# Performance work log

Measured on AMD Instinct MI355X. Metric: run time of the kernel, lower is better.

## Reference

```python
import jax, jax.numpy as jnp
import numpy as np

B, C, IC, H, W = 4, 256, 128, 64, 64
EPS = 1e-5  # BatchNorm eps (eval mode, running stats)


def conv_bn(x, w, b, gamma, beta, mean, var, relu):
    # 1x1 conv == channel contraction; BN in eval mode (affine w/ running stats)
    y = jnp.einsum('oc,bchw->bohw', w, x) + b[None, :, None, None]
    scale = gamma * jax.lax.rsqrt(var + EPS)
    shift = beta - mean * scale
    y = y * scale[None, :, None, None] + shift[None, :, None, None]
    return jax.nn.relu(y) if relu else y


def setup_inputs() -> dict:
    key = jax.random.key(0)
    ks = jax.random.split(key, 32)

    def branch(i, co, ci):
        return dict(
            w=jax.random.normal(ks[i], (co, ci), jnp.float32) * 0.05,
            b=jax.random.normal(ks[i + 1], (co,), jnp.float32) * 0.05,
            gamma=jax.random.uniform(ks[i + 2], (co,), jnp.float32, 0.5, 1.5),
            beta=jax.random.normal(ks[i + 3], (co,), jnp.float32) * 0.05,
            mean=jax.random.normal(ks[i + 4], (co,), jnp.float32) * 0.05,
            var=jax.random.uniform(ks[i + 5], (co,), jnp.float32, 0.5, 1.5),
        )

    g = branch(0, IC, C)
    th = branch(6, IC, C)
    ph = branch(12, IC, C)
    wo = branch(18, C, IC)
    inp = {'x': jax.random.normal(ks[24], (B, C, H, W), jnp.float32)}
    for pre, p in (('g', g), ('th', th), ('ph', ph), ('w', wo)):
        for k, v in p.items():
            inp[f'{pre}_{k}'] = v
    return inp


def reference(x, g_w, g_b, g_gamma, g_beta, g_mean, g_var,
              th_w, th_b, th_gamma, th_beta, th_mean, th_var,
              ph_w, ph_b, ph_gamma, ph_beta, ph_mean, ph_var,
              w_w, w_b, w_gamma, w_beta, w_mean, w_var):
    b, c, h, w = x.shape
    ic = g_w.shape[0]
    g_x = conv_bn(x, g_w, g_b, g_gamma, g_beta, g_mean, g_var, True).reshape(b, ic, h * w)     # [b,ic,n]
    theta = conv_bn(x, th_w, th_b, th_gamma, th_beta, th_mean, th_var, True).reshape(b, ic, h * w)
    phi = conv_bn(x, ph_w, ph_b, ph_gamma, ph_beta, ph_mean, ph_var, True).reshape(b, ic, h * w)
    # unscaled attention over flattened spatial positions
    f = jnp.einsum('bcn,bcm->bnm', theta, phi)     # [b,n,n]
    a = jax.nn.softmax(f, axis=2)
    y = jnp.einsum('bnm,bcm->bcn', a, g_x)         # [b,ic,n]
    y = y.reshape(b, ic, h, w)
    y = conv_bn(y, w_w, w_b, w_gamma, w_beta, w_mean, w_var, False)
    return y + x
```

## Files before the change

### kernel.cpp

```cpp
#include <hip/hip_runtime.h>
#include <math.h>

typedef __attribute__((ext_vector_type(8))) short short8;
typedef __attribute__((ext_vector_type(8))) _Float16 half8;
typedef __attribute__((ext_vector_type(4))) float f32x4;
typedef __attribute__((ext_vector_type(16))) float f32x16;

#define NSP 4096
#define CIN 256
#define ICH 128
#define SPLITS 4
#define TILES_PER_SPLIT 16
#define LOG2E 1.44269504088896f

__device__ __forceinline__ unsigned short f2h(float x){
  union { _Float16 h; unsigned short u; } v; v.h = (_Float16)x; return v.u;
}
__device__ __forceinline__ float h2f(unsigned short u){
  union { _Float16 h; unsigned short u; } v; v.u = u; return (float)v.h;
}
__device__ __forceinline__ unsigned pk2h(float a, float b){
  union { __fp16 __attribute__((ext_vector_type(2))) v; unsigned u; } r;
  r.v = __builtin_amdgcn_cvt_pkrtz(a, b);
  return r.u;
}
__device__ __forceinline__ float fexp2(float x){
  float r;
  asm("v_exp_f32 %0, %1" : "=v"(r) : "v"(x));
  return r;
}
__device__ __forceinline__ int swz(int row, int e){ return e ^ ((row & 7) << 3); }
__device__ __forceinline__ int swzK(int row, int e){ return e ^ ((row & 15) << 3); }

__device__ __forceinline__ f32x4 mfmah(short8 a, short8 b, f32x4 c){
  union { short8 s; half8 h; } ua, ub; ua.s = a; ub.s = b;
  return __builtin_amdgcn_mfma_f32_16x16x32_f16(ua.h, ub.h, c, 0, 0, 0);
}
__device__ __forceinline__ f32x16 mfma32(short8 a, short8 b, f32x16 c){
  union { short8 s; half8 h; } ua, ub; ua.s = a; ub.s = b;
  return __builtin_amdgcn_mfma_f32_32x32x16_f16(ua.h, ub.h, c, 0, 0, 0);
}

__device__ __forceinline__ void st4h(unsigned short* p, unsigned short a, unsigned short b,
                                     unsigned short c, unsigned short d){
  ushort4 v; v.x=a; v.y=b; v.z=c; v.w=d;
  *(ushort4*)p = v;
}

__device__ __forceinline__ void gload_lds16(const unsigned short* g, unsigned short* l){
  __builtin_amdgcn_global_load_lds(
      (const __attribute__((address_space(1))) unsigned int*)g,
      (__attribute__((address_space(3))) unsigned int*)l, 16, 0, 0);
}

__device__ __forceinline__ void stage_nc(const unsigned short* gbase, unsigned short* lds,
                                         int w, int l){
  #pragma unroll
  for (int i=0;i<4;++i){
    int rl = 16*w + 4*i + (l>>4);
    int eg = ((l&15)*8) ^ ((rl&15)<<3);
    gload_lds16(gbase + (size_t)rl*128 + eg, lds + w*2048 + i*512);
  }
}

__device__ __forceinline__ int kperm(int q){
  int m = q & 15;
  return (q & 16) | (((m>>2)&1)<<3) | (m&3) | (((m>>3)&1)<<2);
}

__global__ __launch_bounds__(256) void conv_fused_k(
    const float* __restrict__ x,
    const float* __restrict__ w0, const float* __restrict__ b0,
    const float* __restrict__ ga0, const float* __restrict__ be0,
    const float* __restrict__ me0, const float* __restrict__ va0,
    const float* __restrict__ w1, const float* __restrict__ b1,
    const float* __restrict__ ga1, const float* __restrict__ be1,
    const float* __restrict__ me1, const float* __restrict__ va1,
    const float* __restrict__ w2, const float* __restrict__ b2,
    const float* __restrict__ ga2, const float* __restrict__ be2,
    const float* __restrict__ me2, const float* __restrict__ va2,
    unsigned short* __restrict__ outg, unsigned short* __restrict__ outt,
    unsigned short* __restrict__ outp)
{
  const int b = blockIdx.z, nt = blockIdx.x, ot = blockIdx.y;
  const int n0 = nt*64, o0 = ot*64;
  const int t = threadIdx.x, w = t>>6, l = t&63;
  __shared__ unsigned short xs[64][64];
  __shared__ unsigned short ws[3][64][64];
  __shared__ float sc_s[3][64], sh_s[3][64];
  if (t < 64){
    int o = o0 + t;
    float s0 = ga0[o]*rsqrtf(va0[o]+1e-5f);
    sc_s[0][t]=s0; sh_s[0][t]=be0[o]-me0[o]*s0+b0[o]*s0;
    float s1 = ga1[o]*rsqrtf(va1[o]+1e-5f);
    sc_s[1][t]=s1*LOG2E; sh_s[1][t]=(be1[o]-me1[o]*s1+b1[o]*s1)*LOG2E;
    float s2 = ga2[o]*rsqrtf(va2[o]+1e-5f);
    sc_s[2][t]=s2; sh_s[2][t]=be2[o]-me2[o]*s2+b2[o]*s2;
  }
  const f32x4 Z = {0.f,0.f,0.f,0.f};
  f32x4 acc[3][4];
  #pragma unroll
  for (int br=0;br<3;++br) for (int i=0;i<4;++i) acc[br][i] = Z;
  const float* Wt[3] = {w0, w1, w2};

  for (int kc = 0; kc < CIN; kc += 64){
    __syncthreads();
    #pragma unroll
    for (int p = 0; p < 4; ++p){
      int cw = p*16 + (t>>4);
      int q4 = (t&15)*4;
      float4 xv = *(const float4*)(x + ((size_t)b*CIN + kc + cw)*NSP + n0 + q4);
      float xa[4] = {xv.x, xv.y, xv.z, xv.w};
      #pragma unroll
      for (int i=0;i<4;++i){
        int r = q4 + i;
        xs[r][swz(r, cw)] = f2h(xa[i]);
      }
      #pragma unroll
      for (int br=0;br<3;++br){
        float4 wv = *(const float4*)(Wt[br] + (size_t)(o0 + cw)*CIN + kc + q4);
        int cs = swz(cw, q4);
        st4h(&ws[br][cw][cs], f2h(wv.x), f2h(wv.y), f2h(wv.z), f2h(wv.w));
      }
    }
    __syncthreads();
    #pragma unroll
    for (int kf = 0; kf < 2; ++kf){
      int ko = kf*32 + (l>>4)*8;
      int wr = 16*w + (l&15);
      short8 wf0 = *(const short8*)&ws[0][wr][swz(wr, ko)];
      short8 wf1 = *(const short8*)&ws[1][wr][swz(wr, ko)];
      short8 wf2 = *(const short8*)&ws[2][wr][swz(wr, ko)];
      #pragma unroll
      for (int nf = 0; nf < 4; ++nf){
        int xr = 16*nf + (l&15);
        short8 xf = *(const short8*)&xs[xr][swz(xr, ko)];
        acc[0][nf] = mfmah(wf0, xf, acc[0][nf]);
        acc[1][nf] = mfmah(xf, wf1, acc[1][nf]);
        acc[2][nf] = mfmah(xf, wf2, acc[2][nf]);
      }
    }
  }
  #pragma unroll
  for (int j=0;j<4;++j){
    int ol = 16*w + (l>>4)*4 + j;
    float s = sc_s[0][ol], sh = sh_s[0][ol];
    #pragma unroll
    for (int nf=0;nf<4;++nf){
      int n = n0 + 16*nf + (l&15);
      int nst = (n & ~31) | kperm(n & 31);
      float v = fmaxf(acc[0][nf][j]*s + sh, 0.f);
      outg[((size_t)b*ICH + o0 + ol)*NSP + nst] = f2h(v);
    }
  }
  {
    int ol = 16*w + (l&15);
    float s1 = sc_s[1][ol], sh1 = sh_s[1][ol];
    float s2 = sc_s[2][ol], sh2 = sh_s[2][ol];
    #pragma unroll
    for (int nf=0; nf<4; ++nf)
      #pragma unroll
      for (int j=0;j<4;++j){
        int n = n0 + 16*nf + (l>>4)*4 + j;
        float v1 = fmaxf(acc[1][nf][j]*s1 + sh1, 0.f);
        float v2 = fmaxf(acc[2][nf][j]*s2 + sh2, 0.f);
        outt[((size_t)b*NSP + n)*ICH + o0 + ol] = f2h(v1);
        outp[((size_t)b*NSP + n)*ICH + o0 + ol] = f2h(v2);
      }
  }
}

__global__ __launch_bounds__(256, 2) void attn_k(
  const unsigned short* __restrict__ thp, const unsigned short* __restrict__ php,
  const unsigned short* __restrict__ gb, unsigned short* __restrict__ ypart,
  float* __restrict__ ml)
{
  const int bx = blockIdx.x;
  const int xcd = bx & 7, jj = bx >> 3;
  const int combo = xcd*2 + (jj>>5);
  const int qt = jj & 31;
  const int b = combo & 3, s = combo >> 2;
  const int n0 = qt*128;
  const int t = threadIdx.x, w = t>>6, l = t&63;
  const int hi = l>>5, ln = l&31;

  __shared__ unsigned short kb[2][8192];
  __shared__ unsigned short vb[2][8192];

  stage_nc(thp + ((size_t)b*NSP + n0      )*ICH, &kb[0][0], w, l);
  stage_nc(thp + ((size_t)b*NSP + n0 + 64 )*ICH, &kb[1][0], w, l);
  __syncthreads();
  short8 qf[8];
  {
    const unsigned short* qsrc = (w >> 1) ? &kb[1][0] : &kb[0][0];
    int r = 32*(w & 1) + ln;
    #pragma unroll
    for (int kc=0;kc<8;++kc)
      qf[kc] = *(const short8*)&qsrc[r*128 + swzK(r, kc*16 + 8*hi)];
  }
  __syncthreads();

  f32x16 oa[4];
  #pragma unroll
  for (int i=0;i<4;++i)
    #pragma unroll
    for (int j=0;j<16;++j) oa[i][j] = 0.f;
  float mr = -1e30f, lr = 0.f;
  unsigned pk[16];

  const int tile0 = s*TILES_PER_SPLIT;

  const unsigned short* kp[4];
  const unsigned short* vp[4];
  {
    const unsigned short* kbase = php + ((size_t)b*NSP + tile0*64)*ICH;
    const unsigned short* vbase = gb + (size_t)b*ICH*NSP + tile0*64;
    #pragma unroll
    for (int i=0;i<4;++i){
      int rl = 16*w + 4*i + (l>>4);
      int eg = ((l&15)*8) ^ ((rl&15)<<3);
      kp[i] = kbase + (size_t)rl*128 + eg;
      int cl = 32*w + 8*i + (l>>3);
      int me = ((l&7)*8) ^ ((cl&7)<<3);
      vp[i] = vbase + (size_t)cl*NSP + me;
    }
  }
  {
    unsigned short* kd = &kb[0][0] + w*2048;
    unsigned short* vd = &vb[0][0] + w*2048;
    #pragma unroll
    for (int i=0;i<4;++i){
      gload_lds16(kp[i], kd + i*512); kp[i] += 64*ICH;
      gload_lds16(vp[i], vd + i*512); vp[i] += 64;
    }
  }
  __syncthreads();
  int cur = 0;

  for (int it = 0; it < TILES_PER_SPLIT; ++it){
    if (it < TILES_PER_SPLIT-1){
      unsigned short* kd = &kb[cur^1][0] + w*2048;
      unsigned short* vd = &vb[cur^1][0] + w*2048;
      #pragma unroll
      for (int i=0;i<4;++i){
        gload_lds16(kp[i], kd + i*512); kp[i] += 64*ICH;
        gload_lds16(vp[i], vd + i*512); vp[i] += 64;
      }
    }

    f32x16 sc0, sc1;
    #pragma unroll
    for (int j=0;j<16;++j){ sc0[j]=0.f; sc1[j]=0.f; }
    __builtin_amdgcn_s_setprio(1);
    #pragma unroll
    for (int kc=0;kc<8;++kc){
      int eo = kc*16 + 8*hi;
      short8 a0 = *(const short8*)&kb[cur][(ln     )*128 + swzK(ln,      eo)];
      short8 a1 = *(const short8*)&kb[cur][(32 + ln)*128 + swzK(32 + ln, eo)];
      sc0 = mfma32(a0, qf[kc], sc0);
      sc1 = mfma32(a1, qf[kc], sc1);
    }
    __builtin_amdgcn_s_setprio(0);

    {
      float t0 = fmaxf(fmaxf(sc0[0],sc0[1]),  fmaxf(sc0[2],sc0[3]));
      float t1 = fmaxf(fmaxf(sc0[4],sc0[5]),  fmaxf(sc0[6],sc0[7]));
      float t2 = fmaxf(fmaxf(sc0[8],sc0[9]),  fmaxf(sc0[10],sc0[11]));
      float t3 = fmaxf(fmaxf(sc0[12],sc0[13]),fmaxf(sc0[14],sc0[15]));
      float t4 = fmaxf(fmaxf(sc1[0],sc1[1]),  fmaxf(sc1[2],sc1[3]));
      float t5 = fmaxf(fmaxf(sc1[4],sc1[5]),  fmaxf(sc1[6],sc1[7]));
      float t6 = fmaxf(fmaxf(sc1[8],sc1[9]),  fmaxf(sc1[10],sc1[11]));
      float t7 = fmaxf(fmaxf(sc1[12],sc1[13]),fmaxf(sc1[14],sc1[15]));
      float mx = fmaxf(fmaxf(fmaxf(t0,t1),fmaxf(t2,t3)),
                       fmaxf(fmaxf(t4,t5),fmaxf(t6,t7)));
      mx = fmaxf(mx, __shfl_xor(mx, 32));
      if (__any(mx - mr > 11.5f)){
        float mn = fmaxf(mr, mx);
        float al = fexp2(mr - mn);
        mr = mn; lr *= al;
        #pragma unroll
        for (int j=0;j<16;++j){
          int rowj = (j&3) + 8*(j>>2) + 4*hi;
          float alj = __shfl(al, rowj);
          #pragma unroll
          for (int ct=0;ct<4;++ct) oa[ct][j] *= alj;
        }
      }
      float sA=0.f, sB=0.f, sC=0.f, sD=0.f;
      #pragma unroll
      for (int r=0;r<16;r+=4){
        sc0[r]   = fexp2(sc0[r]  -mr); sA += sc0[r];
        sc0[r+1] = fexp2(sc0[r+1]-mr); sB += sc0[r+1];
        sc0[r+2] = fexp2(sc0[r+2]-mr); sC += sc0[r+2];
        sc0[r+3] = fexp2(sc0[r+3]-mr); sD += sc0[r+3];
      }
      #pragma unroll
      for (int r=0;r<16;r+=4){
        sc1[r]   = fexp2(sc1[r]  -mr); sA += sc1[r];
        sc1[r+1] = fexp2(sc1[r+1]-mr); sB += sc1[r+1];
        sc1[r+2] = fexp2(sc1[r+2]-mr); sC += sc1[r+2];
        sc1[r+3] = fexp2(sc1[r+3]-mr); sD += sc1[r+3];
      }
      lr += (sA + sB) + (sC + sD);
      #pragma unroll
      for (int s2=0;s2<2;++s2)
        #pragma unroll
        for (int q=0;q<4;++q){
          pk[s2*4+q]   = pk2h(sc0[8*s2+2*q], sc0[8*s2+2*q+1]);
          pk[8+s2*4+q] = pk2h(sc1[8*s2+2*q], sc1[8*s2+2*q+1]);
        }
    }

    __builtin_amdgcn_s_setprio(1);
    #pragma unroll
    for (int mt=0;mt<2;++mt)
      #pragma unroll
      for (int s2=0;s2<2;++s2){
        union { unsigned u[4]; short8 s8; } au;
        #pragma unroll
        for (int q=0;q<4;++q) au.u[q] = pk[8*mt+4*s2+q];
        int eo = 32*mt + 16*s2 + 8*hi;
        #pragma unroll
        for (int ct=0;ct<4;++ct){
          int cr = 32*ct + ln;
          short8 bv = *(const short8*)&vb[cur][cr*64 + swz(cr, eo)];
          oa[ct] = mfma32(au.s8, bv, oa[ct]);
        }
      }
    __builtin_amdgcn_s_setprio(0);

    __syncthreads();
    cur ^= 1;
  }

  lr += __shfl_xor(lr, 32);
  float invl = 1.f / lr;
  #pragma unroll
  for (int j=0;j<16;++j){
    int rowj = (j&3) + 8*(j>>2) + 4*hi;
    float invj = __shfl(invl, rowj);
    int n = n0 + 32*w + rowj;
    #pragma unroll
    for (int ct=0;ct<4;++ct){
      int c = 32*ct + ln;
      ypart[(((size_t)s*4 + b)*NSP + n)*ICH + c] = f2h(oa[ct][j]*invj);
    }
  }
  if (l < 32){
    int n = n0 + 32*w + l;
    ml[(((size_t)s*4 + b)*NSP + n)*2 + 0] = mr;
    ml[(((size_t)s*4 + b)*NSP + n)*2 + 1] = lr;
  }
}

__global__ __launch_bounds__(256) void final_k2(
  const unsigned short* __restrict__ ypart, const float* __restrict__ ml,
  const float* __restrict__ x, const float* __restrict__ Wm,
  const float* __restrict__ bias, const float* __restrict__ gamma,
  const float* __restrict__ beta, const float* __restrict__ mean,
  const float* __restrict__ var, float* __restrict__ out)
{
  const int b = blockIdx.z, oth = blockIdx.y, nt = blockIdx.x;
  const int n0 = nt*64, obase = oth*128;
  const int t = threadIdx.x, w = t>>6, l = t&63;
  __shared__ unsigned short ys[64][128];
  __shared__ unsigned short w2s[64][128];
  __shared__ float wc[SPLITS][64];
  __shared__ float sc_s[128], sh_s[128];
  if (t < 128){
    int o = obase + t;
    float s = gamma[o]*rsqrtf(var[o]+1e-5f);
    sc_s[t]=s; sh_s[t]=beta[o]-mean[o]*s+bias[o]*s;
  } else if (t < 192){
    int r = t - 128, n = n0 + r;
    float mv[SPLITS], lv[SPLITS];
    #pragma unroll
    for (int s=0;s<SPLITS;++s){
      mv[s] = ml[(((size_t)s*4 + b)*NSP + n)*2 + 0];
      lv[s] = ml[(((size_t)s*4 + b)*NSP + n)*2 + 1];
    }
    float M = fmaxf(fmaxf(mv[0],mv[1]), fmaxf(mv[2],mv[3]));
    float wsum = 0.f, wv[SPLITS];
    #pragma unroll
    for (int s=0;s<SPLITS;++s){ wv[s] = lv[s]*exp2f(mv[s]-M); wsum += wv[s]; }
    float inv = 1.f/wsum;
    #pragma unroll
    for (int s=0;s<SPLITS;++s) wc[s][r] = wv[s]*inv;
  }
  __syncthreads();
  #pragma unroll
  for (int p=0;p<4;++p){
    int id = p*256 + t, r = id>>4, c8 = (id&15)*8;
    float accv[8] = {0,0,0,0,0,0,0,0};
    #pragma unroll
    for (int s=0;s<SPLITS;++s){
      short8 v = *(const short8*)(ypart + (((size_t)s*4 + b)*NSP + n0 + r)*ICH + c8);
      float wgt = wc[s][r];
      #pragma unroll
      for (int i=0;i<8;++i) accv[i] += wgt * h2f(((unsigned short*)&v)[i]);
    }
    unsigned short hv[8];
    #pragma unroll
    for (int i=0;i<8;++i) hv[i] = f2h(accv[i]);
    *(short8*)&ys[r][swz(r,c8)] = *(short8*)hv;
  }

  const f32x4 Z = {0.f,0.f,0.f,0.f};
  #pragma unroll
  for (int ot2 = 0; ot2 < 2; ++ot2){
    const int o0 = obase + ot2*64;
    #pragma unroll
    for (int p=0;p<4;++p){
      int id = p*256 + t, r = id>>4, c8 = (id&15)*8;
      float4 u0 = *(const float4*)(Wm + (size_t)(o0 + r)*ICH + c8);
      float4 u1 = *(const float4*)(Wm + (size_t)(o0 + r)*ICH + c8 + 4);
      unsigned short wh[8] = {f2h(u0.x),f2h(u0.y),f2h(u0.z),f2h(u0.w),
                              f2h(u1.x),f2h(u1.y),f2h(u1.z),f2h(u1.w)};
      *(short8*)&w2s[r][swz(r,c8)] = *(short8*)wh;
    }
    __syncthreads();
    f32x4 acc[4];
    #pragma unroll
    for (int i=0;i<4;++i) acc[i]=Z;
    #pragma unroll
    for (int kf=0;kf<4;++kf){
      int ko = kf*32 + (l>>4)*8;
      int wr = 16*w + (l&15);
      short8 a = *(const short8*)&w2s[wr][swz(wr,ko)];
      #pragma unroll
      for (int nf=0;nf<4;++nf){
        int yr = 16*nf + (l&15);
        short8 bb = *(const short8*)&ys[yr][swz(yr,ko)];
        acc[nf] = mfmah(a, bb, acc[nf]);
      }
    }
    #pragma unroll
    for (int j=0;j<4;++j){
      int ol = 16*w + (l>>4)*4 + j;
      float s = sc_s[ot2*64 + ol], sh = sh_s[ot2*64 + ol];
      #pragma unroll
      for (int nf=0;nf<4;++nf){
        int n = n0 + 16*nf + (l&15);
        size_t idx = ((size_t)b*CIN + o0 + ol)*NSP + n;
        out[idx] = acc[nf][j]*s + sh + x[idx];
      }
    }
    __syncthreads();
  }
}

extern "C" void kernel_launch(void* const* d_in, const int* in_sizes, int n_in,
                              void* d_out, int out_size, void* d_ws, size_t ws_size,
                              hipStream_t stream){
  const float* x    = (const float*)d_in[0];
  const float* g_w  = (const float*)d_in[1];
  const float* g_b  = (const float*)d_in[2];
  const float* g_ga = (const float*)d_in[3];
  const float* g_be = (const float*)d_in[4];
  const float* g_me = (const float*)d_in[5];
  const float* g_va = (const float*)d_in[6];
  const float* t_w  = (const float*)d_in[7];
  const float* t_b  = (const float*)d_in[8];
  const float* t_ga = (const float*)d_in[9];
  const float* t_be = (const float*)d_in[10];
  const float* t_me = (const float*)d_in[11];
  const float* t_va = (const float*)d_in[12];
  const float* p_w  = (const float*)d_in[13];
  const float* p_b  = (const float*)d_in[14];
  const float* p_ga = (const float*)d_in[15];
  const float* p_be = (const float*)d_in[16];
  const float* p_me = (const float*)d_in[17];
  const float* p_va = (const float*)d_in[18];
  const float* w_w  = (const float*)d_in[19];
  const float* w_b  = (const float*)d_in[20];
  const float* w_ga = (const float*)d_in[21];
  const float* w_be = (const float*)d_in[22];
  const float* w_me = (const float*)d_in[23];
  const float* w_va = (const float*)d_in[24];

  char* ws = (char*)d_ws;
  const size_t SEG = (size_t)4*NSP*ICH*sizeof(unsigned short);
  unsigned short* th_t  = (unsigned short*)(ws);
  unsigned short* ph_t  = (unsigned short*)(ws + SEG);
  unsigned short* g_cn  = (unsigned short*)(ws + 2*SEG);
  unsigned short* ypart = (unsigned short*)(ws + 3*SEG);
  float*          mlb   = (float*)(ws + 3*SEG + SPLITS*SEG);

  dim3 blk(256,1,1);
  conv_fused_k<<<dim3(64,2,4), blk, 0, stream>>>(
      x,
      g_w, g_b, g_ga, g_be, g_me, g_va,
      t_w, t_b, t_ga, t_be, t_me, t_va,
      p_w, p_b, p_ga, p_be, p_me, p_va,
      g_cn, th_t, ph_t);
  attn_k<<<dim3(512,1,1), blk, 0, stream>>>(th_t, ph_t, g_cn, ypart, mlb);
  final_k2<<<dim3(64,2,4), blk, 0, stream>>>(ypart, mlb, x, w_w, w_b, w_ga, w_be, w_me, w_va, (float*)d_out);
}
```

Measured before the change: 70.32 us.

## Interleave softmax exp halves with PV MFMAs and pack fp16 staging stores

```diff
diff --git a/kernel.cpp b/kernel.cpp
--- a/kernel.cpp
+++ b/kernel.cpp
@@ -39,12 +39,6 @@
 __device__ __forceinline__ f32x16 mfma32(short8 a, short8 b, f32x16 c){
   union { short8 s; half8 h; } ua, ub; ua.s = a; ub.s = b;
   return __builtin_amdgcn_mfma_f32_32x32x16_f16(ua.h, ub.h, c, 0, 0, 0);
-}
-
-__device__ __forceinline__ void st4h(unsigned short* p, unsigned short a, unsigned short b,
-                                     unsigned short c, unsigned short d){
-  ushort4 v; v.x=a; v.y=b; v.z=c; v.w=d;
-  *(ushort4*)p = v;
 }
 
 __device__ __forceinline__ void gload_lds16(const unsigned short* g, unsigned short* l){
@@ -106,21 +100,29 @@
   for (int kc = 0; kc < CIN; kc += 64){
     __syncthreads();
     #pragma unroll
+    for (int p2 = 0; p2 < 2; ++p2){
+      int cpr = p2*32 + 2*(t>>4);
+      int nb = (t&15)*4;
+      const float* xr0 = x + ((size_t)b*CIN + kc + cpr)*NSP + n0 + nb;
+      float4 xa = *(const float4*)xr0;
+      float4 xb = *(const float4*)(xr0 + NSP);
+      float aa[4] = {xa.x, xa.y, xa.z, xa.w};
+      float bb[4] = {xb.x, xb.y, xb.z, xb.w};
+      #pragma unroll
+      for (int i=0;i<4;++i){
+        int r = nb + i;
+        *(unsigned*)&xs[r][swz(r, cpr)] = pk2h(aa[i], bb[i]);
+      }
+    }
+    #pragma unroll
     for (int p = 0; p < 4; ++p){
       int cw = p*16 + (t>>4);
       int q4 = (t&15)*4;
-      float4 xv = *(const float4*)(x + ((size_t)b*CIN + kc + cw)*NSP + n0 + q4);
-      float xa[4] = {xv.x, xv.y, xv.z, xv.w};
-      #pragma unroll
-      for (int i=0;i<4;++i){
-        int r = q4 + i;
-        xs[r][swz(r, cw)] = f2h(xa[i]);
-      }
       #pragma unroll
       for (int br=0;br<3;++br){
         float4 wv = *(const float4*)(Wt[br] + (size_t)(o0 + cw)*CIN + kc + q4);
-        int cs = swz(cw, q4);
-        st4h(&ws[br][cw][cs], f2h(wv.x), f2h(wv.y), f2h(wv.z), f2h(wv.w));
+        uint2 u; u.x = pk2h(wv.x, wv.y); u.y = pk2h(wv.z, wv.w);
+        *(uint2*)&ws[br][cw][swz(cw, q4)] = u;
       }
     }
     __syncthreads();
@@ -286,47 +288,63 @@
           for (int ct=0;ct<4;++ct) oa[ct][j] *= alj;
         }
       }
-      float sA=0.f, sB=0.f, sC=0.f, sD=0.f;
-      #pragma unroll
-      for (int r=0;r<16;r+=4){
-        sc0[r]   = fexp2(sc0[r]  -mr); sA += sc0[r];
-        sc0[r+1] = fexp2(sc0[r+1]-mr); sB += sc0[r+1];
-        sc0[r+2] = fexp2(sc0[r+2]-mr); sC += sc0[r+2];
-        sc0[r+3] = fexp2(sc0[r+3]-mr); sD += sc0[r+3];
-      }
-      #pragma unroll
-      for (int r=0;r<16;r+=4){
-        sc1[r]   = fexp2(sc1[r]  -mr); sA += sc1[r];
-        sc1[r+1] = fexp2(sc1[r+1]-mr); sB += sc1[r+1];
-        sc1[r+2] = fexp2(sc1[r+2]-mr); sC += sc1[r+2];
-        sc1[r+3] = fexp2(sc1[r+3]-mr); sD += sc1[r+3];
-      }
-      lr += (sA + sB) + (sC + sD);
-      #pragma unroll
-      for (int s2=0;s2<2;++s2)
-        #pragma unroll
-        for (int q=0;q<4;++q){
-          pk[s2*4+q]   = pk2h(sc0[8*s2+2*q], sc0[8*s2+2*q+1]);
-          pk[8+s2*4+q] = pk2h(sc1[8*s2+2*q], sc1[8*s2+2*q+1]);
-        }
-    }
-
+    }
+
+    float sA=0.f, sB=0.f, sC=0.f, sD=0.f;
+    #pragma unroll
+    for (int r=0;r<16;r+=4){
+      sc0[r]   = fexp2(sc0[r]  -mr); sA += sc0[r];
+      sc0[r+1] = fexp2(sc0[r+1]-mr); sB += sc0[r+1];
+      sc0[r+2] = fexp2(sc0[r+2]-mr); sC += sc0[r+2];
+      sc0[r+3] = fexp2(sc0[r+3]-mr); sD += sc0[r+3];
+    }
+    #pragma unroll
+    for (int s2=0;s2<2;++s2)
+      #pragma unroll
+      for (int q=0;q<4;++q)
+        pk[s2*4+q] = pk2h(sc0[8*s2+2*q], sc0[8*s2+2*q+1]);
     __builtin_amdgcn_s_setprio(1);
     #pragma unroll
-    for (int mt=0;mt<2;++mt)
-      #pragma unroll
-      for (int s2=0;s2<2;++s2){
-        union { unsigned u[4]; short8 s8; } au;
-        #pragma unroll
-        for (int q=0;q<4;++q) au.u[q] = pk[8*mt+4*s2+q];
-        int eo = 32*mt + 16*s2 + 8*hi;
-        #pragma unroll
-        for (int ct=0;ct<4;++ct){
-          int cr = 32*ct + ln;
-          short8 bv = *(const short8*)&vb[cur][cr*64 + swz(cr, eo)];
-          oa[ct] = mfma32(au.s8, bv, oa[ct]);
-        }
-      }
+    for (int s2=0;s2<2;++s2){
+      union { unsigned u[4]; short8 s8; } au;
+      #pragma unroll
+      for (int q=0;q<4;++q) au.u[q] = pk[4*s2+q];
+      int eo = 16*s2 + 8*hi;
+      #pragma unroll
+      for (int ct=0;ct<4;++ct){
+        int cr = 32*ct + ln;
+        short8 bv = *(const short8*)&vb[cur][cr*64 + swz(cr, eo)];
+        oa[ct] = mfma32(au.s8, bv, oa[ct]);
+      }
+    }
+    __builtin_amdgcn_s_setprio(0);
+    #pragma unroll
+    for (int r=0;r<16;r+=4){
+      sc1[r]   = fexp2(sc1[r]  -mr); sA += sc1[r];
+      sc1[r+1] = fexp2(sc1[r+1]-mr); sB += sc1[r+1];
+      sc1[r+2] = fexp2(sc1[r+2]-mr); sC += sc1[r+2];
+      sc1[r+3] = fexp2(sc1[r+3]-mr); sD += sc1[r+3];
+    }
+    #pragma unroll
+    for (int s2=0;s2<2;++s2)
+      #pragma unroll
+      for (int q=0;q<4;++q)
+        pk[8+s2*4+q] = pk2h(sc1[8*s2+2*q], sc1[8*s2+2*q+1]);
+    lr += (sA + sB) + (sC + sD);
+    __builtin_amdgcn_s_setprio(1);
+    #pragma unroll
+    for (int s2=0;s2<2;++s2){
+      union { unsigned u[4]; short8 s8; } au;
+      #pragma unroll
+      for (int q=0;q<4;++q) au.u[q] = pk[8+4*s2+q];
+      int eo = 32 + 16*s2 + 8*hi;
+      #pragma unroll
+      for (int ct=0;ct<4;++ct){
+        int cr = 32*ct + ln;
+        short8 bv = *(const short8*)&vb[cur][cr*64 + swz(cr, eo)];
+        oa[ct] = mfma32(au.s8, bv, oa[ct]);
+      }
+    }
     __builtin_amdgcn_s_setprio(0);
 
     __syncthreads();
```

Result: no change. 69.10 us, median of 2 (-1.7%).
